# Kernel optimization log

Measured on AMD Instinct MI355X. Metric: run time of the kernel, lower is better.

Reference implementation:

```python
import jax, jax.numpy as jnp
import numpy as np

N_NODES = 100000
N_EDGES = 1600000
IN_CH = 1024
FEAT_CH = 128
OUT_CH = 3


def setup_inputs() -> dict:
    key = jax.random.key(0)
    ks = jax.random.split(key, 9)
    features = jax.random.normal(ks[0], (N_NODES, IN_CH), dtype=jnp.float32)
    edges = jax.random.randint(ks[1], (2, N_EDGES), 0, N_NODES, dtype=jnp.int64)
    edges2 = jax.random.randint(ks[2], (2, N_EDGES), 0, N_NODES, dtype=jnp.int64)
    edge_features = jax.random.normal(ks[3], (N_EDGES, 1), dtype=jnp.float32)
    additional_feature = jax.random.normal(ks[4], (N_NODES, 20), dtype=jnp.float32)
    # GCNConv linear weights (glorot-ish scale) and biases
    W1 = jax.random.normal(ks[5], (IN_CH, FEAT_CH), dtype=jnp.float32) * (1.0 / np.sqrt(IN_CH))
    b1 = jnp.zeros((FEAT_CH,), dtype=jnp.float32)
    W2 = jax.random.normal(ks[6], (FEAT_CH, OUT_CH), dtype=jnp.float32) * (1.0 / np.sqrt(FEAT_CH))
    b2 = jnp.zeros((OUT_CH,), dtype=jnp.float32)
    return {"features": features, "edges": edges, "edges2": edges2,
            "edge_features": edge_features, "additional_feature": additional_feature,
            "W1": W1, "b1": b1, "W2": W2, "b2": b2}


def gcn_conv(x, edge_index, W, b, num_nodes):
    """PyG GCNConv: x' = D^{-1/2}(A+I)D^{-1/2} x W + b (self-loops added)."""
    x = x @ W  # project first (cheaper feature dim for aggregation)
    loop = jnp.arange(num_nodes, dtype=edge_index.dtype)
    src = jnp.concatenate([edge_index[0], loop])
    dst = jnp.concatenate([edge_index[1], loop])
    deg = jax.ops.segment_sum(jnp.ones_like(dst, dtype=x.dtype), dst,
                              num_segments=num_nodes)  # >=1 due to self-loops
    dinv = jax.lax.rsqrt(deg)
    norm = dinv[src] * dinv[dst]  # [E+N]
    out = jax.ops.segment_sum(x[src] * norm[:, None], dst, num_segments=num_nodes)
    return out + b


def reference(features, edges, edges2, edge_features, additional_feature, W1, b1, W2, b2):
    # use_additional_channels=False -> features unchanged; edge_features forced to None
    n = features.shape[0]
    x = gcn_conv(features, edges2, W1, b1, n)
    x = jax.nn.relu(x)
    # dropout inactive in eval mode
    return gcn_conv(x, edges2, W2, b2, n)
```

## Files before the change

### kernel.cpp

```cpp
#include <hip/hip_runtime.h>
#include <hip/hip_bf16.h>

typedef __attribute__((ext_vector_type(8))) _Float16 half8;
typedef __attribute__((ext_vector_type(4))) _Float16 half4;
typedef __attribute__((ext_vector_type(4))) float f32x4;

#define N_NODES 100000
#define N_EDGES 1600000
#define IN_CH 1024
#define FEAT 128
#define CAP 64
#define NDIG 196
#define CAPC 10240
#define MROWS 32
#define NGB (N_NODES / MROWS)

__device__ __forceinline__ int swzA(int row, int kbyte) {
    return row * 2048 + (kbyte ^ ((row & 7) << 4) ^ (((kbyte >> 8) & 7) << 4));
}

__global__ void k_prep(const float* __restrict__ W1, _Float16* __restrict__ Bf,
                       int* __restrict__ cursorC, int* __restrict__ done) {
    int idx = blockIdx.x * 256 + threadIdx.x;
    if (idx < IN_CH * FEAT) {
        int col = idx & (FEAT - 1), k = idx >> 7;
        int ct = col >> 4, ks = k >> 5;
        int lane = ((k >> 3) & 3) * 16 + (col & 15);
        int e = k & 7;
        Bf[(((ct * 32 + ks) * 64 + lane) << 3) + e] = (_Float16)W1[idx];
    }
    if (idx < NDIG) cursorC[idx] = idx * CAPC;
    if (idx == 0) *done = 0;
}

__global__ __launch_bounds__(256, 2) void k_build_gemm(
    const float* __restrict__ A, const _Float16* __restrict__ Bf,
    const int4* __restrict__ src4, const int4* __restrict__ dst4,
    int* __restrict__ cursorC, uint2* __restrict__ recs,
    int* __restrict__ csr, int* __restrict__ cnt, float* __restrict__ dinvarr,
    int* __restrict__ done, _Float16* __restrict__ H, int M, int e4)
{
    __shared__ union {
        _Float16 As[MROWS * IN_CH];
        struct { int hist[NDIG], segoff[NDIG], lcur[NDIG]; } bin;
        int cl[512];
    } sm;
    const int t = threadIdx.x;

    if (blockIdx.x < NDIG) {
        const int b = blockIdx.x;
        if (t < NDIG) sm.bin.hist[t] = 0;
        __syncthreads();
        const int base4 = b * 2048;
        int4 sv[8], dv[8];
#pragma unroll
        for (int j = 0; j < 8; ++j) {
            int idx = base4 + j * 256 + t;
            if (idx < e4) { sv[j] = src4[idx]; dv[j] = dst4[idx]; }
            else { sv[j] = (int4){-1,-1,-1,-1}; dv[j] = (int4){-1,-1,-1,-1}; }
        }
#pragma unroll
        for (int j = 0; j < 8; ++j) {
            int dd[4] = {dv[j].x, dv[j].y, dv[j].z, dv[j].w};
            int ss[4] = {sv[j].x, sv[j].y, sv[j].z, sv[j].w};
#pragma unroll
            for (int c = 0; c < 4; ++c)
                if ((unsigned)dd[c] < N_NODES && (unsigned)ss[c] < N_NODES)
                    atomicAdd(&sm.bin.hist[dd[c] >> 9], 1);
        }
        __syncthreads();
        if (t < NDIG) {
            sm.bin.segoff[t] = atomicAdd(&cursorC[t], sm.bin.hist[t]);
            sm.bin.lcur[t] = 0;
        }
        __syncthreads();
#pragma unroll
        for (int j = 0; j < 8; ++j) {
            int dd[4] = {dv[j].x, dv[j].y, dv[j].z, dv[j].w};
            int ss[4] = {sv[j].x, sv[j].y, sv[j].z, sv[j].w};
#pragma unroll
            for (int c = 0; c < 4; ++c) {
                if ((unsigned)dd[c] < N_NODES && (unsigned)ss[c] < N_NODES) {
                    int dg = dd[c] >> 9;
                    int r = atomicAdd(&sm.bin.lcur[dg], 1);
                    int pos = sm.bin.segoff[dg] + r;
                    if (pos < (dg + 1) * CAPC)
                        recs[pos] = (uint2){(unsigned)ss[c], (unsigned)dd[c]};
                }
            }
        }
        __syncthreads();
        if (t == 0) {
            __threadfence();
            __hip_atomic_fetch_add(done, 1, __ATOMIC_RELEASE, __HIP_MEMORY_SCOPE_AGENT);
            while (__hip_atomic_load(done, __ATOMIC_ACQUIRE, __HIP_MEMORY_SCOPE_AGENT) < NDIG)
                __builtin_amdgcn_s_sleep(8);
        }
        __syncthreads();
        const int d = blockIdx.x;
        for (int j = t; j < 512; j += 256) sm.cl[j] = 0;
        __syncthreads();
        const int base = d * CAPC;
        int n = cursorC[d] - base;
        if (n > CAPC) n = CAPC;
        for (int k = t; k < n; k += 256) {
            uint2 r = recs[base + k];
            int local = (int)r.y & 511;
            int slot = atomicAdd(&sm.cl[local], 1);
            if (slot < CAP) csr[((int)r.y << 6) + slot] = (int)r.x;
        }
        __syncthreads();
        const int node0 = d << 9;
        for (int j = t; j < 512; j += 256) {
            int node = node0 + j;
            if (node < N_NODES) {
                int c = sm.cl[j] < CAP ? sm.cl[j] : CAP;
                cnt[node] = c;
                dinvarr[node] = rsqrtf((float)(c + 1));
            }
        }
        return;
    }

    const int gb = blockIdx.x - NDIG;
    const int brow0 = gb * MROWS;
    const int wid = t >> 6, lane = t & 63;

    {
        const int row = t >> 3;
        const int c0 = (t & 7) * 128;
        int grow = brow0 + row; if (grow >= M) grow = M - 1;
        const float* pa = A + (size_t)grow * IN_CH + c0;
#pragma unroll
        for (int ch = 0; ch < 4; ++ch) {
            float4 v[8];
#pragma unroll
            for (int j = 0; j < 8; ++j) v[j] = *(const float4*)(pa + ch * 32 + j * 4);
#pragma unroll
            for (int j = 0; j < 8; ++j) {
                half4 h;
                h[0] = (_Float16)v[j].x; h[1] = (_Float16)v[j].y;
                h[2] = (_Float16)v[j].z; h[3] = (_Float16)v[j].w;
                int kbyte = (c0 + ch * 32 + j * 4) * 2;
                *(half4*)((char*)sm.As + swzA(row, kbyte)) = h;
            }
        }
    }
    __syncthreads();

    const int rt = wid >> 1;
    const int ctb = (wid & 1) * 4;
    const int arow = rt * 16 + (lane & 15);
    const int asub = (lane >> 4) * 16;

    f32x4 acc[4];
#pragma unroll
    for (int c = 0; c < 4; ++c) acc[c] = (f32x4){0.f, 0.f, 0.f, 0.f};

    const _Float16* bfl = Bf + lane * 8;

#pragma unroll 4
    for (int ks = 0; ks < 32; ++ks) {
        half8 a = *(const half8*)((char*)sm.As + swzA(arow, ks * 64 + asub));
        half8 b0 = *(const half8*)(bfl + (((ctb + 0) * 32 + ks) << 9));
        half8 b1 = *(const half8*)(bfl + (((ctb + 1) * 32 + ks) << 9));
        half8 b2 = *(const half8*)(bfl + (((ctb + 2) * 32 + ks) << 9));
        half8 b3 = *(const half8*)(bfl + (((ctb + 3) * 32 + ks) << 9));
        acc[0] = __builtin_amdgcn_mfma_f32_16x16x32_f16(a, b0, acc[0], 0, 0, 0);
        acc[1] = __builtin_amdgcn_mfma_f32_16x16x32_f16(a, b1, acc[1], 0, 0, 0);
        acc[2] = __builtin_amdgcn_mfma_f32_16x16x32_f16(a, b2, acc[2], 0, 0, 0);
        acc[3] = __builtin_amdgcn_mfma_f32_16x16x32_f16(a, b3, acc[3], 0, 0, 0);
    }

    {
        int colb = lane & 15, rgrp = (lane >> 4) * 4;
#pragma unroll
        for (int c = 0; c < 4; ++c) {
            int gcol = (ctb + c) * 16 + colb;
#pragma unroll
            for (int r = 0; r < 4; ++r) {
                int grow = brow0 + rt * 16 + rgrp + r;
                if (grow < M) H[(size_t)grow * FEAT + gcol] = (_Float16)acc[c][r];
            }
        }
    }
}

__global__ __launch_bounds__(256) void k_agg1(const _Float16* __restrict__ H,
                                              const int* __restrict__ csr,
                                              const int* __restrict__ cnt,
                                              const float* __restrict__ dinvarr,
                                              const float* __restrict__ b1,
                                              const float* __restrict__ W2,
                                              float* __restrict__ Y, int n) {
    int wid = threadIdx.x >> 6, lane = threadIdx.x & 63;
    int i = blockIdx.x * 4 + wid;
    if (i >= n) return;
    const int g = lane >> 4, u = lane & 15;
    int m = cnt[i];
    float di = dinvarr[i];

    int sl; float dl;
    if (lane < m) { sl = csr[(i << 6) + lane]; dl = dinvarr[sl]; }
    else          { sl = i;                    dl = (lane == m) ? di : 0.f; }
    int mm = (m < 63 ? m : 63) + 1;

    float ax[8];
#pragma unroll
    for (int j = 0; j < 8; ++j) ax[j] = 0.f;

    for (int e = 0; e < mm; e += 16) {
        int idx0 = e + g, idx1 = e + 4 + g, idx2 = e + 8 + g, idx3 = e + 12 + g;
        bool v0 = idx0 < mm, v1 = idx1 < mm, v2 = idx2 < mm, v3 = idx3 < mm;
        int c0i = v0 ? idx0 : 0, c1i = v1 ? idx1 : 0;
        int c2i = v2 ? idx2 : 0, c3i = v3 ? idx3 : 0;
        int s0 = __shfl(sl, c0i); float w0 = __shfl(dl, c0i);
        int s1 = __shfl(sl, c1i); float w1 = __shfl(dl, c1i);
        int s2 = __shfl(sl, c2i); float w2 = __shfl(dl, c2i);
        int s3 = __shfl(sl, c3i); float w3 = __shfl(dl, c3i);
        if (!v0) { s0 = i; w0 = 0.f; }
        if (!v1) { s1 = i; w1 = 0.f; }
        if (!v2) { s2 = i; w2 = 0.f; }
        if (!v3) { s3 = i; w3 = 0.f; }
        half8 h0 = *(const half8*)(H + ((size_t)s0 << 7) + u * 8);
        half8 h1 = *(const half8*)(H + ((size_t)s1 << 7) + u * 8);
        half8 h2 = *(const half8*)(H + ((size_t)s2 << 7) + u * 8);
        half8 h3 = *(const half8*)(H + ((size_t)s3 << 7) + u * 8);
#pragma unroll
        for (int j = 0; j < 8; ++j)
            ax[j] += w0 * (float)h0[j] + w1 * (float)h1[j]
                   + w2 * (float)h2[j] + w3 * (float)h3[j];
    }

#pragma unroll
    for (int j = 0; j < 8; ++j) {
        ax[j] += __shfl_xor(ax[j], 16);
        ax[j] += __shfl_xor(ax[j], 32);
    }

    int c0 = u * 8;
    float y0 = 0.f, y1 = 0.f, y2 = 0.f;
#pragma unroll
    for (int j = 0; j < 8; ++j) {
        float x = di * ax[j] + b1[c0 + j];
        x = x > 0.f ? x : 0.f;
        y0 += x * W2[(c0 + j) * 3 + 0];
        y1 += x * W2[(c0 + j) * 3 + 1];
        y2 += x * W2[(c0 + j) * 3 + 2];
    }
#pragma unroll
    for (int d = 1; d < 16; d <<= 1) {
        y0 += __shfl_xor(y0, d);
        y1 += __shfl_xor(y1, d);
        y2 += __shfl_xor(y2, d);
    }
    if (lane == 0) {
        float* yp = Y + (size_t)i * 4;
        yp[0] = di * y0; yp[1] = di * y1; yp[2] = di * y2;
    }
}

__global__ void k_agg2(const float* __restrict__ Y, const int* __restrict__ csr,
                       const int* __restrict__ cnt, const float* __restrict__ dinvarr,
                       const float* __restrict__ b2, float* __restrict__ out, int n) {
    int i = blockIdx.x * 256 + threadIdx.x;
    if (i >= n) return;
    int m = cnt[i];
    float di = dinvarr[i];
    int base = i << 6;
    const float4* Y4 = (const float4*)Y;
    float4 self = Y4[i];
    float a0 = self.x, a1 = self.y, a2 = self.z;
    int e = 0;
    for (; e + 3 < m; e += 4) {
        int s0 = csr[base + e],     s1 = csr[base + e + 1];
        int s2 = csr[base + e + 2], s3 = csr[base + e + 3];
        float4 v0 = Y4[s0], v1 = Y4[s1], v2 = Y4[s2], v3 = Y4[s3];
        a0 += (v0.x + v1.x) + (v2.x + v3.x);
        a1 += (v0.y + v1.y) + (v2.y + v3.y);
        a2 += (v0.z + v1.z) + (v2.z + v3.z);
    }
    for (; e < m; ++e) {
        float4 v0 = Y4[csr[base + e]];
        a0 += v0.x; a1 += v0.y; a2 += v0.z;
    }
    out[(size_t)i * 3 + 0] = di * a0 + b2[0];
    out[(size_t)i * 3 + 1] = di * a1 + b2[1];
    out[(size_t)i * 3 + 2] = di * a2 + b2[2];
}

extern "C" void kernel_launch(void* const* d_in, const int* in_sizes, int n_in,
                              void* d_out, int out_size, void* d_ws, size_t ws_size,
                              hipStream_t stream) {
    const float* features = (const float*)d_in[0];
    const int* edges2 = (const int*)d_in[2];
    const float* W1 = (const float*)d_in[5];
    const float* b1 = (const float*)d_in[6];
    const float* W2 = (const float*)d_in[7];
    const float* b2 = (const float*)d_in[8];
    float* out = (float*)d_out;

    const int N = N_NODES, E = N_EDGES;
    const int4* src4 = (const int4*)edges2;
    const int4* dst4 = (const int4*)(edges2 + E);
    int e4 = E / 4;

    char* p = (char*)d_ws;
    auto carve = [&](size_t bytes) { char* q = p; p += (bytes + 255) & ~(size_t)255; return q; };
    int* cnt       = (int*)carve(4 * (size_t)N);
    float* dinvarr = (float*)carve(4 * (size_t)N);
    int* cursorC   = (int*)carve(4 * NDIG);
    int* done      = (int*)carve(4);
    uint2* recs    = (uint2*)carve(8 * (size_t)NDIG * CAPC);
    int* csr       = (int*)carve(4 * (size_t)N * CAP);
    _Float16* Bf   = (_Float16*)carve(2 * (size_t)IN_CH * FEAT);
    _Float16* H    = (_Float16*)carve(2 * (size_t)N * FEAT);
    float* Y       = (float*)carve(16 * (size_t)N);

    k_prep<<<dim3(512), dim3(256), 0, stream>>>(W1, Bf, cursorC, done);
    k_build_gemm<<<dim3(NDIG + NGB), dim3(256), 0, stream>>>(
        features, Bf, src4, dst4, cursorC, recs, csr, cnt, dinvarr, done, H, N, e4);
    k_agg1<<<dim3((N + 3) / 4), dim3(256), 0, stream>>>(H, csr, cnt, dinvarr, b1, W2, Y, N);
    k_agg2<<<dim3((N + 255) / 256), dim3(256), 0, stream>>>(Y, csr, cnt, dinvarr, b2, out, N);
}
```

Before: 302.6 us.

## Halve GEMM row tile to 16 and raise occupancy with B-fragment prefetch

```diff
diff --git a/kernel.cpp b/kernel.cpp
--- a/kernel.cpp
+++ b/kernel.cpp
@@ -12,7 +12,7 @@
 #define CAP 64
 #define NDIG 196
 #define CAPC 10240
-#define MROWS 32
+#define MROWS 16
 #define NGB (N_NODES / MROWS)
 
 __device__ __forceinline__ int swzA(int row, int kbyte) {
@@ -33,7 +33,7 @@
     if (idx == 0) *done = 0;
 }
 
-__global__ __launch_bounds__(256, 2) void k_build_gemm(
+__global__ __launch_bounds__(256, 4) void k_build_gemm(
     const float* __restrict__ A, const _Float16* __restrict__ Bf,
     const int4* __restrict__ src4, const int4* __restrict__ dst4,
     int* __restrict__ cursorC, uint2* __restrict__ recs,
@@ -127,61 +127,68 @@
     const int wid = t >> 6, lane = t & 63;
 
     {
-        const int row = t >> 3;
-        const int c0 = (t & 7) * 128;
-        int grow = brow0 + row; if (grow >= M) grow = M - 1;
-        const float* pa = A + (size_t)grow * IN_CH + c0;
-#pragma unroll
-        for (int ch = 0; ch < 4; ++ch) {
-            float4 v[8];
-#pragma unroll
-            for (int j = 0; j < 8; ++j) v[j] = *(const float4*)(pa + ch * 32 + j * 4);
-#pragma unroll
-            for (int j = 0; j < 8; ++j) {
-                half4 h;
-                h[0] = (_Float16)v[j].x; h[1] = (_Float16)v[j].y;
-                h[2] = (_Float16)v[j].z; h[3] = (_Float16)v[j].w;
-                int kbyte = (c0 + ch * 32 + j * 4) * 2;
-                *(half4*)((char*)sm.As + swzA(row, kbyte)) = h;
-            }
+        const int row = t >> 4;
+        const int c0 = (t & 15) * 64;
+        const float* pa = A + (size_t)(brow0 + row) * IN_CH + c0;
+        float4 v0[8], v1[8];
+#pragma unroll
+        for (int j = 0; j < 8; ++j) v0[j] = *(const float4*)(pa + j * 4);
+#pragma unroll
+        for (int j = 0; j < 8; ++j) v1[j] = *(const float4*)(pa + 32 + j * 4);
+#pragma unroll
+        for (int j = 0; j < 4; ++j) {
+            half8 h;
+            h[0] = (_Float16)v0[2 * j].x;     h[1] = (_Float16)v0[2 * j].y;
+            h[2] = (_Float16)v0[2 * j].z;     h[3] = (_Float16)v0[2 * j].w;
+            h[4] = (_Float16)v0[2 * j + 1].x; h[5] = (_Float16)v0[2 * j + 1].y;
+            h[6] = (_Float16)v0[2 * j + 1].z; h[7] = (_Float16)v0[2 * j + 1].w;
+            *(half8*)((char*)sm.As + swzA(row, c0 * 2 + j * 16)) = h;
+        }
+#pragma unroll
+        for (int j = 0; j < 4; ++j) {
+            half8 h;
+            h[0] = (_Float16)v1[2 * j].x;     h[1] = (_Float16)v1[2 * j].y;
+            h[2] = (_Float16)v1[2 * j].z;     h[3] = (_Float16)v1[2 * j].w;
+            h[4] = (_Float16)v1[2 * j + 1].x; h[5] = (_Float16)v1[2 * j + 1].y;
+            h[6] = (_Float16)v1[2 * j + 1].z; h[7] = (_Float16)v1[2 * j + 1].w;
+            *(half8*)((char*)sm.As + swzA(row, (c0 + 32) * 2 + j * 16)) = h;
         }
     }
     __syncthreads();
 
-    const int rt = wid >> 1;
-    const int ctb = (wid & 1) * 4;
-    const int arow = rt * 16 + (lane & 15);
+    const int ct0 = wid * 2, ct1 = wid * 2 + 1;
+    const _Float16* bfl = Bf + lane * 8;
+    const _Float16* pb0 = bfl + ((size_t)(ct0 * 32) << 9);
+    const _Float16* pb1 = bfl + ((size_t)(ct1 * 32) << 9);
+    const int arow = lane & 15;
     const int asub = (lane >> 4) * 16;
 
-    f32x4 acc[4];
-#pragma unroll
-    for (int c = 0; c < 4; ++c) acc[c] = (f32x4){0.f, 0.f, 0.f, 0.f};
-
-    const _Float16* bfl = Bf + lane * 8;
-
+    f32x4 acc0 = (f32x4){0.f, 0.f, 0.f, 0.f};
+    f32x4 acc1 = (f32x4){0.f, 0.f, 0.f, 0.f};
+
+    half8 bc0 = *(const half8*)(pb0);
+    half8 bc1 = *(const half8*)(pb1);
 #pragma unroll 4
     for (int ks = 0; ks < 32; ++ks) {
+        half8 bn0 = bc0, bn1 = bc1;
+        if (ks < 31) {
+            bn0 = *(const half8*)(pb0 + ((size_t)(ks + 1) << 9));
+            bn1 = *(const half8*)(pb1 + ((size_t)(ks + 1) << 9));
+        }
         half8 a = *(const half8*)((char*)sm.As + swzA(arow, ks * 64 + asub));
-        half8 b0 = *(const half8*)(bfl + (((ctb + 0) * 32 + ks) << 9));
-        half8 b1 = *(const half8*)(bfl + (((ctb + 1) * 32 + ks) << 9));
-        half8 b2 = *(const half8*)(bfl + (((ctb + 2) * 32 + ks) << 9));
-        half8 b3 = *(const half8*)(bfl + (((ctb + 3) * 32 + ks) << 9));
-        acc[0] = __builtin_amdgcn_mfma_f32_16x16x32_f16(a, b0, acc[0], 0, 0, 0);
-        acc[1] = __builtin_amdgcn_mfma_f32_16x16x32_f16(a, b1, acc[1], 0, 0, 0);
-        acc[2] = __builtin_amdgcn_mfma_f32_16x16x32_f16(a, b2, acc[2], 0, 0, 0);
-        acc[3] = __builtin_amdgcn_mfma_f32_16x16x32_f16(a, b3, acc[3], 0, 0, 0);
+        acc0 = __builtin_amdgcn_mfma_f32_16x16x32_f16(a, bc0, acc0, 0, 0, 0);
+        acc1 = __builtin_amdgcn_mfma_f32_16x16x32_f16(a, bc1, acc1, 0, 0, 0);
+        bc0 = bn0; bc1 = bn1;
     }
 
     {
         int colb = lane & 15, rgrp = (lane >> 4) * 4;
 #pragma unroll
-        for (int c = 0; c < 4; ++c) {
-            int gcol = (ctb + c) * 16 + colb;
-#pragma unroll
-            for (int r = 0; r < 4; ++r) {
-                int grow = brow0 + rt * 16 + rgrp + r;
-                if (grow < M) H[(size_t)grow * FEAT + gcol] = (_Float16)acc[c][r];
-            }
+        for (int r = 0; r < 4; ++r) {
+            int grow = brow0 + rgrp + r;
+            _Float16* hp = H + (size_t)grow * FEAT;
+            hp[ct0 * 16 + colb] = (_Float16)acc0[r];
+            hp[ct1 * 16 + colb] = (_Float16)acc1[r];
         }
     }
 }
```

New measurement: 297.2 us. About the same (-1.8%).

## Double-buffer GEMM A tiles via async global-to-LDS loads with larger row tiles

Applied to the files above, without the earlier changes.

```diff
diff --git a/kernel.cpp b/kernel.cpp
--- a/kernel.cpp
+++ b/kernel.cpp
@@ -2,7 +2,6 @@
 #include <hip/hip_bf16.h>
 
 typedef __attribute__((ext_vector_type(8))) _Float16 half8;
-typedef __attribute__((ext_vector_type(4))) _Float16 half4;
 typedef __attribute__((ext_vector_type(4))) float f32x4;
 
 #define N_NODES 100000
@@ -12,11 +11,12 @@
 #define CAP 64
 #define NDIG 196
 #define CAPC 10240
-#define MROWS 32
-#define NGB (N_NODES / MROWS)
-
-__device__ __forceinline__ int swzA(int row, int kbyte) {
-    return row * 2048 + (kbyte ^ ((row & 7) << 4) ^ (((kbyte >> 8) & 7) << 4));
+#define NGB ((N_NODES + 127) / 128)
+
+__device__ __forceinline__ void gload16(const void* g, void* l) {
+    __builtin_amdgcn_global_load_lds(
+        (const __attribute__((address_space(1))) unsigned int*)g,
+        (__attribute__((address_space(3))) unsigned int*)l, 16, 0, 0);
 }
 
 __global__ void k_prep(const float* __restrict__ W1, _Float16* __restrict__ Bf,
@@ -24,10 +24,10 @@
     int idx = blockIdx.x * 256 + threadIdx.x;
     if (idx < IN_CH * FEAT) {
         int col = idx & (FEAT - 1), k = idx >> 7;
-        int ct = col >> 4, ks = k >> 5;
+        int cf = col >> 4, s = k >> 5;
         int lane = ((k >> 3) & 3) * 16 + (col & 15);
         int e = k & 7;
-        Bf[(((ct * 32 + ks) * 64 + lane) << 3) + e] = (_Float16)W1[idx];
+        Bf[(((cf * 32 + s) * 64 + lane) << 3) + e] = (_Float16)W1[idx];
     }
     if (idx < NDIG) cursorC[idx] = idx * CAPC;
     if (idx == 0) *done = 0;
@@ -41,7 +41,7 @@
     int* __restrict__ done, _Float16* __restrict__ H, int M, int e4)
 {
     __shared__ union {
-        _Float16 As[MROWS * IN_CH];
+        float As[2][8192];
         struct { int hist[NDIG], segoff[NDIG], lcur[NDIG]; } bin;
         int cl[512];
     } sm;
@@ -123,64 +123,100 @@
     }
 
     const int gb = blockIdx.x - NDIG;
-    const int brow0 = gb * MROWS;
+    const int brow0 = gb << 7;
     const int wid = t >> 6, lane = t & 63;
 
-    {
-        const int row = t >> 3;
-        const int c0 = (t & 7) * 128;
-        int grow = brow0 + row; if (grow >= M) grow = M - 1;
-        const float* pa = A + (size_t)grow * IN_CH + c0;
-#pragma unroll
-        for (int ch = 0; ch < 4; ++ch) {
-            float4 v[8];
-#pragma unroll
-            for (int j = 0; j < 8; ++j) v[j] = *(const float4*)(pa + ch * 32 + j * 4);
-#pragma unroll
-            for (int j = 0; j < 8; ++j) {
-                half4 h;
-                h[0] = (_Float16)v[j].x; h[1] = (_Float16)v[j].y;
-                h[2] = (_Float16)v[j].z; h[3] = (_Float16)v[j].w;
-                int kbyte = (c0 + ch * 32 + j * 4) * 2;
-                *(half4*)((char*)sm.As + swzA(row, kbyte)) = h;
-            }
-        }
-    }
+    const char* gsrc[8];
+#pragma unroll
+    for (int i = 0; i < 8; ++i) {
+        int R = (wid * 8 + i) * 4 + (lane >> 4);
+        int grow = brow0 + R; if (grow >= M) grow = M - 1;
+        int gcol = ((lane & 15) * 16) ^ ((R & 15) << 4);
+        gsrc[i] = (const char*)A + (size_t)grow * 4096 + gcol;
+    }
+
+#define STAGE(buf, kt)                                                          \
+    {                                                                           \
+        _Pragma("unroll") for (int i = 0; i < 8; ++i)                           \
+            gload16(gsrc[i] + (kt) * 256,                                       \
+                    (char*)sm.As[buf] + (wid * 8 + i) * 1024);                  \
+    }
+#define LOADB(dst, s)                                                           \
+    {                                                                           \
+        _Pragma("unroll") for (int cf = 0; cf < 8; ++cf)                        \
+            dst[cf] = *(const half8*)(Bf + (((cf * 32 + (s)) << 9)) + lane * 8);\
+    }
+#define AFRAG(dst, cur, rf, kk)                                                 \
+    {                                                                           \
+        int R_ = wid * 32 + (rf) * 16 + (lane & 15);                            \
+        int k0_ = (kk) * 128 + (lane >> 4) * 32;                                \
+        int sw_ = (R_ & 15) << 4;                                               \
+        f32x4 lo_ = *(const f32x4*)((char*)sm.As[cur] + R_ * 256 + (k0_ ^ sw_));\
+        f32x4 hi_ = *(const f32x4*)((char*)sm.As[cur] + R_ * 256 + ((k0_ + 16) ^ sw_)); \
+        dst[0] = (_Float16)lo_.x; dst[1] = (_Float16)lo_.y;                     \
+        dst[2] = (_Float16)lo_.z; dst[3] = (_Float16)lo_.w;                     \
+        dst[4] = (_Float16)hi_.x; dst[5] = (_Float16)hi_.y;                     \
+        dst[6] = (_Float16)hi_.z; dst[7] = (_Float16)hi_.w;                     \
+    }
+
+    f32x4 acc[2][8];
+#pragma unroll
+    for (int rf = 0; rf < 2; ++rf)
+#pragma unroll
+        for (int cf = 0; cf < 8; ++cf) acc[rf][cf] = (f32x4){0.f, 0.f, 0.f, 0.f};
+
+    half8 bbA[8], bbB[8];
+    STAGE(0, 0);
+    LOADB(bbA, 0);
     __syncthreads();
 
-    const int rt = wid >> 1;
-    const int ctb = (wid & 1) * 4;
-    const int arow = rt * 16 + (lane & 15);
-    const int asub = (lane >> 4) * 16;
-
-    f32x4 acc[4];
-#pragma unroll
-    for (int c = 0; c < 4; ++c) acc[c] = (f32x4){0.f, 0.f, 0.f, 0.f};
-
-    const _Float16* bfl = Bf + lane * 8;
-
-#pragma unroll 4
-    for (int ks = 0; ks < 32; ++ks) {
-        half8 a = *(const half8*)((char*)sm.As + swzA(arow, ks * 64 + asub));
-        half8 b0 = *(const half8*)(bfl + (((ctb + 0) * 32 + ks) << 9));
-        half8 b1 = *(const half8*)(bfl + (((ctb + 1) * 32 + ks) << 9));
-        half8 b2 = *(const half8*)(bfl + (((ctb + 2) * 32 + ks) << 9));
-        half8 b3 = *(const half8*)(bfl + (((ctb + 3) * 32 + ks) << 9));
-        acc[0] = __builtin_amdgcn_mfma_f32_16x16x32_f16(a, b0, acc[0], 0, 0, 0);
-        acc[1] = __builtin_amdgcn_mfma_f32_16x16x32_f16(a, b1, acc[1], 0, 0, 0);
-        acc[2] = __builtin_amdgcn_mfma_f32_16x16x32_f16(a, b2, acc[2], 0, 0, 0);
-        acc[3] = __builtin_amdgcn_mfma_f32_16x16x32_f16(a, b3, acc[3], 0, 0, 0);
-    }
+    int cur = 0;
+#pragma unroll 1
+    for (int kt = 0; kt < 16; ++kt) {
+        if (kt < 15) STAGE(cur ^ 1, kt + 1);
+        const int s = kt * 2;
+        LOADB(bbB, s + 1);
+        {
+            half8 a0, a1;
+            AFRAG(a0, cur, 0, 0);
+            AFRAG(a1, cur, 1, 0);
+#pragma unroll
+            for (int cf = 0; cf < 8; ++cf) {
+                acc[0][cf] = __builtin_amdgcn_mfma_f32_16x16x32_f16(a0, bbA[cf], acc[0][cf], 0, 0, 0);
+                acc[1][cf] = __builtin_amdgcn_mfma_f32_16x16x32_f16(a1, bbA[cf], acc[1][cf], 0, 0, 0);
+            }
+        }
+        if (s + 2 < 32) LOADB(bbA, s + 2);
+        {
+            half8 a0, a1;
+            AFRAG(a0, cur, 0, 1);
+            AFRAG(a1, cur, 1, 1);
+#pragma unroll
+            for (int cf = 0; cf < 8; ++cf) {
+                acc[0][cf] = __builtin_amdgcn_mfma_f32_16x16x32_f16(a0, bbB[cf], acc[0][cf], 0, 0, 0);
+                acc[1][cf] = __builtin_amdgcn_mfma_f32_16x16x32_f16(a1, bbB[cf], acc[1][cf], 0, 0, 0);
+            }
+        }
+        __syncthreads();
+        cur ^= 1;
+    }
+#undef STAGE
+#undef LOADB
+#undef AFRAG
 
     {
         int colb = lane & 15, rgrp = (lane >> 4) * 4;
 #pragma unroll
-        for (int c = 0; c < 4; ++c) {
-            int gcol = (ctb + c) * 16 + colb;
+        for (int rf = 0; rf < 2; ++rf) {
 #pragma unroll
             for (int r = 0; r < 4; ++r) {
-                int grow = brow0 + rt * 16 + rgrp + r;
-                if (grow < M) H[(size_t)grow * FEAT + gcol] = (_Float16)acc[c][r];
+                int grow = brow0 + wid * 32 + rf * 16 + rgrp + r;
+                if (grow < M) {
+                    _Float16* hp = H + (size_t)grow * FEAT + colb;
+#pragma unroll
+                    for (int cf = 0; cf < 8; ++cf)
+                        hp[cf * 16] = (_Float16)acc[rf][cf][r];
+                }
             }
         }
     }
```

Result: faster. 244.6 us (-19.2%).
